# Kernel optimization log

Hardware: AMD Instinct MI355X
Metric: run time of the kernel (lower is better)

Reference implementation:

```python
import jax, jax.numpy as jnp
import numpy as np

N_CODEBOOKS = 4
N_EMBED = 1024
EMBED_DIM = 64
PATCH = 4
BETA = 0.25
EPS = 1e-5
USAGE_W = 0.01


def setup_inputs() -> dict:
    key = jax.random.key(0)
    k1, k2 = jax.random.split(key)
    z = jax.random.normal(k1, (8, 64, 128, 128), dtype=jnp.float32)
    # one EMA codebook per quantizer, initialized ~ randn like torch buffer
    codebooks = jax.random.normal(k2, (N_CODEBOOKS, N_EMBED, EMBED_DIM), dtype=jnp.float32)
    return {"z": z, "codebooks": codebooks}


def _usage_loss(indices, n_embed):
    # negative-entropy penalty on code usage (no gradient path: counts are ints)
    counts = jnp.bincount(indices.reshape(-1), length=n_embed).astype(jnp.float32)
    probs = (counts + EPS) / (counts.sum() + EPS * n_embed)
    entropy = -jnp.sum(probs * jnp.log(probs + EPS))
    return jnp.log(jnp.float32(n_embed)) - entropy


def _ema_quantize(residual, embedding):
    # residual: [N, C, ph, pw], embedding: [n_e, C]; eval mode (no EMA buffer update)
    N, C, ph, pw = residual.shape
    z_flat = residual.transpose(0, 2, 3, 1).reshape(-1, C)  # [M, C]
    d = (jnp.sum(z_flat ** 2, axis=1, keepdims=True)
         + jnp.sum(embedding ** 2, axis=1)
         - 2.0 * z_flat @ embedding.T)  # [M, n_e]
    idx = jnp.argmin(d, axis=1)  # [M]
    z_q = embedding[idx].reshape(N, ph, pw, C).transpose(0, 3, 1, 2)  # [N, C, ph, pw]
    loss = BETA * jnp.mean((jax.lax.stop_gradient(z_q) - residual) ** 2)
    z_q_st = residual + jax.lax.stop_gradient(z_q - residual)  # straight-through
    return z_q_st, loss, idx.reshape(N, ph, pw)


def reference(z, codebooks):
    B, C, H, W = z.shape
    h, w = H // PATCH, W // PATCH
    # b c (h ph) (w pw) -> (b h w) c ph pw
    zp = (z.reshape(B, C, h, PATCH, w, PATCH)
            .transpose(0, 2, 4, 1, 3, 5)
            .reshape(B * h * w, C, PATCH, PATCH))
    zq_acc = jnp.zeros_like(zp)
    residual = zp
    losses, all_idx = [], []
    for i in range(N_CODEBOOKS):
        zq_i, loss_i, idx_i = _ema_quantize(residual, codebooks[i])
        loss_i = loss_i + USAGE_W * _usage_loss(idx_i, N_EMBED)
        zq_acc = zq_acc + zq_i
        residual = residual - zq_i
        losses.append(loss_i)
        all_idx.append(idx_i.reshape(idx_i.shape[0], -1))  # [N, ph*pw]
    loss = jnp.stack(losses).sum()
    # (b h w) c ph pw -> b c (h ph) (w pw)
    z_q = (zq_acc.reshape(B, h, w, C, PATCH, PATCH)
                 .transpose(0, 3, 1, 4, 2, 5)
                 .reshape(B, C, H, W))
    # [N, patch_area, n_codebooks] -> [b, h, w, patch_area, n_codebooks]
    min_idx = jnp.stack(all_idx, axis=-1).reshape(B, h, w, PATCH * PATCH, N_CODEBOOKS)
    return z_q, loss, min_idx
```

## Files before the change

kernel.cpp:

```cpp
#include <hip/hip_runtime.h>
#include <math.h>

typedef __attribute__((ext_vector_type(8))) short short8;
typedef __attribute__((ext_vector_type(4))) float f32x4;

#define NCB 4
#define NE 1024
#define DIM 64
#define HW 16384
#define NPIX 131072
#define NWAVES 4096
#define MSE_DENOM 8388608.0f
#define EPSF 1e-5f
#define CHUNK_BYTES 24576
#define CHUNK_SHORTS 12288
#define NCHUNK 16

__device__ __forceinline__ unsigned short f2bf(float x) {
    unsigned u = __float_as_uint(x);
    u += 0x7fffu + ((u >> 16) & 1u);
    return (unsigned short)(u >> 16);
}
__device__ __forceinline__ float bf2f(unsigned short h) {
    return __uint_as_float(((unsigned)h) << 16);
}

__global__ __launch_bounds__(64) void rvq_norms(const float* __restrict__ cb,
                                                float* __restrict__ nrmh) {
    int code = blockIdx.x * 64 + threadIdx.x;
    const float4* row = reinterpret_cast<const float4*>(cb + (size_t)code * DIM);
    float s0 = 0.f, s1 = 0.f, s2 = 0.f, s3 = 0.f;
#pragma unroll
    for (int k = 0; k < 16; ++k) {
        float4 v = row[k];
        s0 = fmaf(v.x, v.x, s0); s1 = fmaf(v.y, v.y, s1);
        s2 = fmaf(v.z, v.z, s2); s3 = fmaf(v.w, v.w, s3);
    }
    nrmh[code] = -0.5f * ((s0 + s1) + (s2 + s3));
}

__global__ __launch_bounds__(256) void rvq_presplit(const float* __restrict__ cb,
                                                    unsigned short* __restrict__ gB) {
    int blk = blockIdx.x;
    int tid = threadIdx.x;
    int code = tid >> 2, dg = tid & 3;
    int c0 = (blk & 15) << 6;
    int i  = blk >> 4;
    const float4* s4 = reinterpret_cast<const float4*>(
        cb + ((size_t)i * NE + c0 + code) * DIM + dg * 16);
    float v[16];
    {
        float4 q;
        q = s4[0]; v[0]=q.x; v[1]=q.y; v[2]=q.z; v[3]=q.w;
        q = s4[1]; v[4]=q.x; v[5]=q.y; v[6]=q.z; v[7]=q.w;
        q = s4[2]; v[8]=q.x; v[9]=q.y; v[10]=q.z; v[11]=q.w;
        q = s4[3]; v[12]=q.x; v[13]=q.y; v[14]=q.z; v[15]=q.w;
    }
    char* outc = reinterpret_cast<char*>(gB + (size_t)blk * CHUNK_SHORTS);
    int linbase = code * 128 + dg * 32;
    int sw = (code & 7) << 4;
#pragma unroll
    for (int h = 0; h < 2; ++h) {
        short8 p1, p2, p3;
#pragma unroll
        for (int e = 0; e < 8; ++e) {
            float t = v[h * 8 + e];
            unsigned short u1 = f2bf(t); t -= bf2f(u1);
            unsigned short u2 = f2bf(t); t -= bf2f(u2);
            unsigned short u3 = f2bf(t);
            p1[e] = (short)u1; p2[e] = (short)u2; p3[e] = (short)u3;
        }
        int a = (linbase + h * 16) ^ sw;
        *reinterpret_cast<short8*>(outc + a)         = p1;
        *reinterpret_cast<short8*>(outc + 8192 + a)  = p2;
        *reinterpret_cast<short8*>(outc + 16384 + a) = p3;
    }
}

__device__ __forceinline__ void gload16(const void* gsrc, void* ldst) {
    __builtin_amdgcn_global_load_lds(
        (const __attribute__((address_space(1))) unsigned int*)gsrc,
        (__attribute__((address_space(3))) unsigned int*)ldst, 16, 0, 0);
}

__global__ __launch_bounds__(256, 2) void rvq_main(
    const float* __restrict__ z, const unsigned short* __restrict__ gB,
    const float* __restrict__ nrmh, const float* __restrict__ cb,
    float* __restrict__ out_zq, float* __restrict__ out_idx,
    unsigned* __restrict__ hist, float* __restrict__ msePartial)
{
    __shared__ uint4 sB[3][CHUNK_BYTES / 16];
    __shared__ int   sBest[4][32];

    const int tid  = threadIdx.x;
    const int lane = tid & 63;
    const int wid  = tid >> 6;
    const int col  = lane & 15;
    const int g    = lane >> 4;
    const int blockPix = blockIdx.x * 128;
    char* sBase = reinterpret_cast<char*>(sB);
    const int sw = (col & 7) << 4;

    size_t zb[2];
#pragma unroll
    for (int m = 0; m < 2; ++m) {
        int pf = blockPix + wid * 32 + m * 16 + col;
        zb[m] = (size_t)(pf >> 14) * 1048576 + (size_t)(pf & 16383);
    }

    float r[2][2][8];
#pragma unroll
    for (int m = 0; m < 2; ++m)
#pragma unroll
        for (int kh = 0; kh < 2; ++kh)
#pragma unroll
            for (int e = 0; e < 8; ++e)
                r[m][kh][e] = z[zb[m] + (size_t)(kh * 32 + g * 8 + e) * HW];

    for (int i = 0; i < NCB; ++i) {
        const char* gBi = reinterpret_cast<const char*>(gB) + (size_t)i * NCHUNK * CHUNK_BYTES;
        const float* nrm_i = nrmh + i * NE;

        short8 A[3][2][2];
#pragma unroll
        for (int m = 0; m < 2; ++m)
#pragma unroll
            for (int kh = 0; kh < 2; ++kh)
#pragma unroll
                for (int e = 0; e < 8; ++e) {
                    float t = r[m][kh][e];
                    unsigned short u1 = f2bf(t); t -= bf2f(u1);
                    unsigned short u2 = f2bf(t); t -= bf2f(u2);
                    unsigned short u3 = f2bf(t);
                    A[0][m][kh][e] = (short)u1;
                    A[1][m][kh][e] = (short)u2;
                    A[2][m][kh][e] = (short)u3;
                }

#pragma unroll
        for (int k = 0; k < 6; ++k)
            gload16(gBi + k * 4096 + tid * 16, sBase + k * 4096 + tid * 16);

        float maxv[2][4]; int maxi[2][4];
#pragma unroll
        for (int m = 0; m < 2; ++m)
#pragma unroll
            for (int rr = 0; rr < 4; ++rr) { maxv[m][rr] = -3.4e38f; maxi[m][rr] = 0; }

        for (int c = 0; c < NCHUNK; ++c) {
            if (c < NCHUNK - 1) {
                const char* gc = gBi + (size_t)(c + 1) * CHUNK_BYTES;
                char* sbn = sBase + ((c + 1) % 3) * CHUNK_BYTES;
#pragma unroll
                for (int k = 0; k < 6; ++k)
                    gload16(gc + k * 4096 + tid * 16, sbn + k * 4096 + tid * 16);
                asm volatile("s_waitcnt vmcnt(6)" ::: "memory");
            } else {
                asm volatile("s_waitcnt vmcnt(0)" ::: "memory");
            }
            __builtin_amdgcn_s_barrier();
            const char* sbc = sBase + (c % 3) * CHUNK_BYTES;

#pragma unroll
            for (int sub = 0; sub < 4; ++sub) {
                const int code = (sub << 4) + col;
                float nh = nrm_i[(c << 6) + code];
                f32x4 acc[2];
#pragma unroll
                for (int rr = 0; rr < 4; ++rr) { acc[0][rr] = nh; acc[1][rr] = nh; }

                __builtin_amdgcn_s_setprio(1);
#pragma unroll
                for (int sb = 0; sb < 3; ++sb) {
                    short8 B0 = *reinterpret_cast<const short8*>(
                        sbc + sb * 8192 + ((((code << 7) + (g << 4))) ^ sw));
                    short8 B1 = *reinterpret_cast<const short8*>(
                        sbc + sb * 8192 + ((((code << 7) + 64 + (g << 4))) ^ sw));
#pragma unroll
                    for (int sa = 0; sa < 3 - sb; ++sa) {
                        acc[0] = __builtin_amdgcn_mfma_f32_16x16x32_bf16(A[sa][0][0], B0, acc[0], 0, 0, 0);
                        acc[1] = __builtin_amdgcn_mfma_f32_16x16x32_bf16(A[sa][1][0], B0, acc[1], 0, 0, 0);
                        acc[0] = __builtin_amdgcn_mfma_f32_16x16x32_bf16(A[sa][0][1], B1, acc[0], 0, 0, 0);
                        acc[1] = __builtin_amdgcn_mfma_f32_16x16x32_bf16(A[sa][1][1], B1, acc[1], 0, 0, 0);
                    }
                }
                __builtin_amdgcn_s_setprio(0);

#pragma unroll
                for (int m = 0; m < 2; ++m)
#pragma unroll
                    for (int rr = 0; rr < 4; ++rr) {
                        float s = acc[m][rr];
                        if (s > maxv[m][rr]) { maxv[m][rr] = s; maxi[m][rr] = (c << 6) + code; }
                    }
            }
        }

#pragma unroll
        for (int m = 0; m < 2; ++m)
#pragma unroll
            for (int rr = 0; rr < 4; ++rr) {
                float v = maxv[m][rr]; int ix = maxi[m][rr];
#pragma unroll
                for (int off = 1; off < 16; off <<= 1) {
                    float ov = __shfl_xor(v, off, 64);
                    int   oi = __shfl_xor(ix, off, 64);
                    if (ov > v || (ov == v && oi < ix)) { v = ov; ix = oi; }
                }
                maxi[m][rr] = ix;
            }
        if (col == 0) {
#pragma unroll
            for (int m = 0; m < 2; ++m)
#pragma unroll
                for (int rr = 0; rr < 4; ++rr)
                    sBest[wid][m * 16 + g * 4 + rr] = maxi[m][rr];
        }

        const float* cbi = cb + (size_t)i * NE * DIM;
        if (lane < 16) {
#pragma unroll
            for (int m = 0; m < 2; ++m) {
                int pfr = blockPix + wid * 32 + m * 16 + lane;
                int bb = pfr >> 14, yy = (pfr >> 7) & 127, xx = pfr & 127;
                int bi = sBest[wid][m * 16 + lane];
                size_t off = (size_t)bb * 65536 + (size_t)(yy >> 2) * 2048
                           + (size_t)(xx >> 2) * 64
                           + (size_t)(((yy & 3) << 2) + (xx & 3)) * 4 + (size_t)i;
                out_idx[off] = (float)bi;
                atomicAdd(&hist[i * NE + bi], 1u);
            }
        }

#pragma unroll
        for (int m = 0; m < 2; ++m) {
            const int best = sBest[wid][m * 16 + col];
            const float* er = cbi + (size_t)best * DIM;
#pragma unroll
            for (int kh = 0; kh < 2; ++kh) {
                const float4* e4 = reinterpret_cast<const float4*>(er + kh * 32 + g * 8);
                float4 q0 = e4[0], q1 = e4[1];
                r[m][kh][0] -= q0.x; r[m][kh][1] -= q0.y;
                r[m][kh][2] -= q0.z; r[m][kh][3] -= q0.w;
                r[m][kh][4] -= q1.x; r[m][kh][5] -= q1.y;
                r[m][kh][6] -= q1.z; r[m][kh][7] -= q1.w;
            }
        }

        float s = 0.f;
#pragma unroll
        for (int m = 0; m < 2; ++m)
#pragma unroll
            for (int kh = 0; kh < 2; ++kh)
#pragma unroll
                for (int e = 0; e < 8; ++e) s = fmaf(r[m][kh][e], r[m][kh][e], s);
#pragma unroll
        for (int d_ = 32; d_ > 0; d_ >>= 1) s += __shfl_down(s, d_, 64);
        if (lane == 0) msePartial[i * NWAVES + blockIdx.x * 4 + wid] = s;

        __syncthreads();
    }

#pragma unroll
    for (int m = 0; m < 2; ++m)
#pragma unroll
        for (int kh = 0; kh < 2; ++kh)
#pragma unroll
            for (int e = 0; e < 8; ++e) {
                size_t o = zb[m] + (size_t)(kh * 32 + g * 8 + e) * HW;
                out_zq[o] = z[o] - r[m][kh][e];
            }
}

__global__ __launch_bounds__(1024) void rvq_finalize(
    const unsigned* __restrict__ hist, const float* __restrict__ msePartial,
    float* __restrict__ out_loss)
{
    __shared__ float red[1024];
    int t = threadIdx.x;
    float loss = 0.f;
    for (int i = 0; i < NCB; ++i) {
        float cnt = (float)hist[i * NE + t];
        float prob = (cnt + EPSF) / (131072.0f + EPSF * 1024.0f);
        red[t] = -prob * logf(prob + EPSF);
        __syncthreads();
        for (int s = 512; s > 0; s >>= 1) { if (t < s) red[t] += red[t + s]; __syncthreads(); }
        float entropy = red[0];
        __syncthreads();
        float acc = 0.f;
#pragma unroll
        for (int k = 0; k < 4; ++k) acc += msePartial[i * NWAVES + k * 1024 + t];
        red[t] = acc;
        __syncthreads();
        for (int s = 512; s > 0; s >>= 1) { if (t < s) red[t] += red[t + s]; __syncthreads(); }
        float mse_sum = red[0];
        __syncthreads();
        loss += 0.25f * (mse_sum / MSE_DENOM) + 0.01f * (logf(1024.0f) - entropy);
    }
    if (t == 0) out_loss[0] = loss;
}

extern "C" void kernel_launch(void* const* d_in, const int* in_sizes, int n_in,
                              void* d_out, int out_size, void* d_ws, size_t ws_size,
                              hipStream_t stream) {
    const float* z  = (const float*)d_in[0];
    const float* cb = (const float*)d_in[1];

    float* out      = (float*)d_out;
    float* out_zq   = out;
    float* out_loss = out + 8388608;
    float* out_idx  = out + 8388609;

    unsigned* hist        = (unsigned*)d_ws;
    float*    nrmh        = (float*)((char*)d_ws + 16384);
    float*    msePartial  = (float*)((char*)d_ws + 32768);
    unsigned short* gB    = (unsigned short*)((char*)d_ws + 163840);

    hipMemsetAsync(d_ws, 0, 16384, stream);
    rvq_norms<<<64, 64, 0, stream>>>(cb, nrmh);
    rvq_presplit<<<64, 256, 0, stream>>>(cb, gB);
    rvq_main<<<1024, 256, 0, stream>>>(z, gB, nrmh, cb, out_zq, out_idx, hist, msePartial);
    rvq_finalize<<<1, 1024, 0, stream>>>(hist, msePartial, out_loss);
}
```

Baseline: 384.6 us.

## Give each wave its own LDS codebook stream and drop block barriers

Switches from a block-shared triple-buffered codebook chunk, guarded by s_barrier, to a per-wave double buffer of 16-code chunks, so waves stream the codebook independently with no block-level synchronization. Norm vectors are prefetched into per-wave LDS, and the next codebook is prefetched at the end of each stage. The aim is to remove barrier stalls between waves. In exchange, each wave now fetches the whole codebook itself, roughly quadrupling L2-to-LDS traffic per block, and the prefetch depth per wave is shallow.

Measured after the change: 491.1 us. 27.7% more time.

```diff
diff --git a/kernel.cpp b/kernel.cpp
--- a/kernel.cpp
+++ b/kernel.cpp
@@ -12,9 +12,8 @@
 #define NWAVES 4096
 #define MSE_DENOM 8388608.0f
 #define EPSF 1e-5f
-#define CHUNK_BYTES 24576
-#define CHUNK_SHORTS 12288
-#define NCHUNK 16
+#define WCB 6144
+#define NWC 64
 
 __device__ __forceinline__ unsigned short f2bf(float x) {
     unsigned u = __float_as_uint(x);
@@ -43,11 +42,12 @@
                                                     unsigned short* __restrict__ gB) {
     int blk = blockIdx.x;
     int tid = threadIdx.x;
-    int code = tid >> 2, dg = tid & 3;
+    int code64 = tid >> 2, dg = tid & 3;
     int c0 = (blk & 15) << 6;
     int i  = blk >> 4;
+    int C  = c0 + code64;
     const float4* s4 = reinterpret_cast<const float4*>(
-        cb + ((size_t)i * NE + c0 + code) * DIM + dg * 16);
+        cb + ((size_t)i * NE + C) * DIM + dg * 16);
     float v[16];
     {
         float4 q;
@@ -56,9 +56,10 @@
         q = s4[2]; v[8]=q.x; v[9]=q.y; v[10]=q.z; v[11]=q.w;
         q = s4[3]; v[12]=q.x; v[13]=q.y; v[14]=q.z; v[15]=q.w;
     }
-    char* outc = reinterpret_cast<char*>(gB + (size_t)blk * CHUNK_SHORTS);
-    int linbase = code * 128 + dg * 32;
-    int sw = (code & 7) << 4;
+    char* outc = reinterpret_cast<char*>(gB) + ((size_t)i * NWC + (C >> 4)) * WCB;
+    int j = C & 15;
+    int linbase = j * 128 + dg * 32;
+    int sw = (j & 7) << 4;
 #pragma unroll
     for (int h = 0; h < 2; ++h) {
         short8 p1, p2, p3;
@@ -71,9 +72,9 @@
             p1[e] = (short)u1; p2[e] = (short)u2; p3[e] = (short)u3;
         }
         int a = (linbase + h * 16) ^ sw;
-        *reinterpret_cast<short8*>(outc + a)         = p1;
-        *reinterpret_cast<short8*>(outc + 8192 + a)  = p2;
-        *reinterpret_cast<short8*>(outc + 16384 + a) = p3;
+        *reinterpret_cast<short8*>(outc + a)        = p1;
+        *reinterpret_cast<short8*>(outc + 2048 + a) = p2;
+        *reinterpret_cast<short8*>(outc + 4096 + a) = p3;
     }
 }
 
@@ -89,7 +90,8 @@
     float* __restrict__ out_zq, float* __restrict__ out_idx,
     unsigned* __restrict__ hist, float* __restrict__ msePartial)
 {
-    __shared__ uint4 sB[3][CHUNK_BYTES / 16];
+    __shared__ char  sW[4 * 2 * WCB];
+    __shared__ float sNh[4][NE];
     __shared__ int   sBest[4][32];
 
     const int tid  = threadIdx.x;
@@ -98,8 +100,18 @@
     const int col  = lane & 15;
     const int g    = lane >> 4;
     const int blockPix = blockIdx.x * 128;
-    char* sBase = reinterpret_cast<char*>(sB);
+    char* myBuf = sW + wid * (2 * WCB);
+    char* myNh  = reinterpret_cast<char*>(&sNh[wid][0]);
     const int sw = (col & 7) << 4;
+    const char* gBb = reinterpret_cast<const char*>(gB);
+
+#pragma unroll
+    for (int k = 0; k < 4; ++k)
+        gload16(reinterpret_cast<const char*>(nrmh) + k * 1024 + lane * 16,
+                myNh + k * 1024 + lane * 16);
+#pragma unroll
+    for (int k = 0; k < 6; ++k)
+        gload16(gBb + k * 1024 + lane * 16, myBuf + k * 1024 + lane * 16);
 
     size_t zb[2];
 #pragma unroll
@@ -118,8 +130,7 @@
                 r[m][kh][e] = z[zb[m] + (size_t)(kh * 32 + g * 8 + e) * HW];
 
     for (int i = 0; i < NCB; ++i) {
-        const char* gBi = reinterpret_cast<const char*>(gB) + (size_t)i * NCHUNK * CHUNK_BYTES;
-        const float* nrm_i = nrmh + i * NE;
+        const char* gBi = gBb + (size_t)i * NWC * WCB;
 
         short8 A[3][2][2];
 #pragma unroll
@@ -137,63 +148,66 @@
                     A[2][m][kh][e] = (short)u3;
                 }
 
-#pragma unroll
-        for (int k = 0; k < 6; ++k)
-            gload16(gBi + k * 4096 + tid * 16, sBase + k * 4096 + tid * 16);
-
         float maxv[2][4]; int maxi[2][4];
 #pragma unroll
         for (int m = 0; m < 2; ++m)
 #pragma unroll
             for (int rr = 0; rr < 4; ++rr) { maxv[m][rr] = -3.4e38f; maxi[m][rr] = 0; }
 
-        for (int c = 0; c < NCHUNK; ++c) {
-            if (c < NCHUNK - 1) {
-                const char* gc = gBi + (size_t)(c + 1) * CHUNK_BYTES;
-                char* sbn = sBase + ((c + 1) % 3) * CHUNK_BYTES;
+        for (int c = 0; c < NWC; ++c) {
+            if (c < NWC - 1) {
+                const char* gc = gBi + (size_t)(c + 1) * WCB;
+                char* dst = myBuf + ((c + 1) & 1) * WCB;
 #pragma unroll
                 for (int k = 0; k < 6; ++k)
-                    gload16(gc + k * 4096 + tid * 16, sbn + k * 4096 + tid * 16);
+                    gload16(gc + k * 1024 + lane * 16, dst + k * 1024 + lane * 16);
                 asm volatile("s_waitcnt vmcnt(6)" ::: "memory");
             } else {
                 asm volatile("s_waitcnt vmcnt(0)" ::: "memory");
             }
-            __builtin_amdgcn_s_barrier();
-            const char* sbc = sBase + (c % 3) * CHUNK_BYTES;
-
-#pragma unroll
-            for (int sub = 0; sub < 4; ++sub) {
-                const int code = (sub << 4) + col;
-                float nh = nrm_i[(c << 6) + code];
-                f32x4 acc[2];
-#pragma unroll
-                for (int rr = 0; rr < 4; ++rr) { acc[0][rr] = nh; acc[1][rr] = nh; }
-
-                __builtin_amdgcn_s_setprio(1);
-#pragma unroll
-                for (int sb = 0; sb < 3; ++sb) {
-                    short8 B0 = *reinterpret_cast<const short8*>(
-                        sbc + sb * 8192 + ((((code << 7) + (g << 4))) ^ sw));
-                    short8 B1 = *reinterpret_cast<const short8*>(
-                        sbc + sb * 8192 + ((((code << 7) + 64 + (g << 4))) ^ sw));
-#pragma unroll
-                    for (int sa = 0; sa < 3 - sb; ++sa) {
-                        acc[0] = __builtin_amdgcn_mfma_f32_16x16x32_bf16(A[sa][0][0], B0, acc[0], 0, 0, 0);
-                        acc[1] = __builtin_amdgcn_mfma_f32_16x16x32_bf16(A[sa][1][0], B0, acc[1], 0, 0, 0);
-                        acc[0] = __builtin_amdgcn_mfma_f32_16x16x32_bf16(A[sa][0][1], B1, acc[0], 0, 0, 0);
-                        acc[1] = __builtin_amdgcn_mfma_f32_16x16x32_bf16(A[sa][1][1], B1, acc[1], 0, 0, 0);
-                    }
+            const char* sbc = myBuf + (c & 1) * WCB;
+
+            const int code = col;
+            float nh = sNh[wid][(c << 4) + col];
+            f32x4 acc[2];
+#pragma unroll
+            for (int rr = 0; rr < 4; ++rr) { acc[0][rr] = nh; acc[1][rr] = nh; }
+
+            __builtin_amdgcn_s_setprio(1);
+#pragma unroll
+            for (int sb = 0; sb < 3; ++sb) {
+                short8 B0 = *reinterpret_cast<const short8*>(
+                    sbc + sb * 2048 + ((((code << 7) + (g << 4))) ^ sw));
+                short8 B1 = *reinterpret_cast<const short8*>(
+                    sbc + sb * 2048 + ((((code << 7) + 64 + (g << 4))) ^ sw));
+#pragma unroll
+                for (int sa = 0; sa < 3 - sb; ++sa) {
+                    acc[0] = __builtin_amdgcn_mfma_f32_16x16x32_bf16(A[sa][0][0], B0, acc[0], 0, 0, 0);
+                    acc[1] = __builtin_amdgcn_mfma_f32_16x16x32_bf16(A[sa][1][0], B0, acc[1], 0, 0, 0);
+                    acc[0] = __builtin_amdgcn_mfma_f32_16x16x32_bf16(A[sa][0][1], B1, acc[0], 0, 0, 0);
+                    acc[1] = __builtin_amdgcn_mfma_f32_16x16x32_bf16(A[sa][1][1], B1, acc[1], 0, 0, 0);
                 }
-                __builtin_amdgcn_s_setprio(0);
-
-#pragma unroll
-                for (int m = 0; m < 2; ++m)
-#pragma unroll
-                    for (int rr = 0; rr < 4; ++rr) {
-                        float s = acc[m][rr];
-                        if (s > maxv[m][rr]) { maxv[m][rr] = s; maxi[m][rr] = (c << 6) + code; }
-                    }
-            }
+            }
+            __builtin_amdgcn_s_setprio(0);
+
+#pragma unroll
+            for (int m = 0; m < 2; ++m)
+#pragma unroll
+                for (int rr = 0; rr < 4; ++rr) {
+                    float s = acc[m][rr];
+                    if (s > maxv[m][rr]) { maxv[m][rr] = s; maxi[m][rr] = (c << 4) + code; }
+                }
+        }
+
+        if (i < NCB - 1) {
+            const char* nsrc = reinterpret_cast<const char*>(nrmh) + (size_t)(i + 1) * 4096;
+#pragma unroll
+            for (int k = 0; k < 4; ++k)
+                gload16(nsrc + k * 1024 + lane * 16, myNh + k * 1024 + lane * 16);
+            const char* gn = gBb + (size_t)(i + 1) * NWC * WCB;
+#pragma unroll
+            for (int k = 0; k < 6; ++k)
+                gload16(gn + k * 1024 + lane * 16, myBuf + k * 1024 + lane * 16);
         }
 
 #pragma unroll
@@ -257,8 +271,6 @@
 #pragma unroll
         for (int d_ = 32; d_ > 0; d_ >>= 1) s += __shfl_down(s, d_, 64);
         if (lane == 0) msePartial[i * NWAVES + blockIdx.x * 4 + wid] = s;
-
-        __syncthreads();
     }
 
 #pragma unroll
```
